# Optimization experiments

Hardware: AMD Instinct MI355X
Metric: run time of the kernel (lower is better)

## Reference

```python
import jax, jax.numpy as jnp
import numpy as np


def setup_inputs() -> dict:
    key = jax.random.key(0)
    ks = jax.random.split(key, 7)
    N, E, D_IN, D_OUT = 50000, 800000, 128, 128
    features = jax.random.normal(ks[0], (N, D_IN), dtype=jnp.float32)
    src = jax.random.randint(ks[1], (E,), 0, N, dtype=jnp.int64)
    dst = jax.random.randint(ks[2], (E,), 0, N, dtype=jnp.int64)
    W1 = jax.random.normal(ks[3], (D_OUT, D_IN), dtype=jnp.float32) * (1.0 / np.sqrt(D_IN))
    b1 = jax.random.normal(ks[4], (D_OUT,), dtype=jnp.float32) * 0.01
    W2 = jax.random.normal(ks[5], (1, 2 * D_OUT), dtype=jnp.float32) * (1.0 / np.sqrt(2 * D_OUT))
    b2 = jax.random.normal(ks[6], (1,), dtype=jnp.float32) * 0.01
    return {"features": features, "src": src, "dst": dst,
            "W1": W1, "b1": b1, "W2": W2, "b2": b2}


def reference(features, src, dst, W1, b1, W2, b2):
    # Gather endpoint features per edge: [E, D_in]
    f_src = features[src]
    f_dst = features[dst]
    # Shared linear projection (torch Linear: x @ W.T + b) -> [E, D_out]
    h_src = jnp.einsum('ed,od->eo', f_src, W1) + b1
    h_dst = jnp.einsum('ed,od->eo', f_dst, W1) + b1
    # Concat [diff, sum] -> [E, 2*D_out]; dropout is identity at inference
    e_feats = jnp.concatenate([h_src - h_dst, h_src + h_dst], axis=1)
    # Final linear to scalar per edge, squeeze, tanh -> [E]
    out = jnp.tanh((jnp.einsum('ef,of->eo', e_feats, W2) + b2).squeeze(-1))
    return out
```

## Files before the change

kernel.cpp:

```cpp
#include <hip/hip_runtime.h>
#include <math.h>

#define D 128


__global__ void prep_kernel(const float* __restrict__ W1, const float* __restrict__ b1,
                            const float* __restrict__ W2, const float* __restrict__ b2,
                            float* __restrict__ uvc) {
    __shared__ float su[4 * D];
    __shared__ float sv[4 * D];
    __shared__ float sc[D];
    int tid = threadIdx.x;
    int d = tid & (D - 1);
    int ch = tid >> 7;
    float u = 0.f, v = 0.f;
    int o0 = ch * 32;
    #pragma unroll 8
    for (int k = 0; k < 32; ++k) {
        int o = o0 + k;
        float wa = W2[o];
        float wb = W2[D + o];
        float w1 = W1[o * D + d];
        u += (wa + wb) * w1;
        v += (wb - wa) * w1;
    }
    su[ch * D + d] = u;
    sv[ch * D + d] = v;
    if (ch == 0) sc[d] = 2.f * W2[D + d] * b1[d];
    __syncthreads();
    if (tid < D) {
        float uu = su[d] + su[D + d] + su[2 * D + d] + su[3 * D + d];
        float vv = sv[d] + sv[D + d] + sv[2 * D + d] + sv[3 * D + d];
        uvc[2 * d]     = uu;
        uvc[2 * d + 1] = vv;
    } else if (tid == D) {
        float cc = b2[0];
        for (int o = 0; o < D; ++o) cc += sc[o];
        uvc[2 * D] = cc;
    }
}

__global__ void node_kernel(const float* __restrict__ feat, const float* __restrict__ uvc,
                            float2* __restrict__ st, int N) {
    int wave = (int)((blockIdx.x * blockDim.x + threadIdx.x) >> 6);
    int lane = threadIdx.x & 63;
    int half = lane >> 5;
    int l = lane & 31;
    int node = wave * 2 + half;
    if (node >= N) return;
    float4 f = ((const float4*)(feat + (size_t)node * D))[l];
    float4 a = ((const float4*)uvc)[2 * l];
    float4 b = ((const float4*)uvc)[2 * l + 1];
    float s = f.x * a.x + f.y * a.z + f.z * b.x + f.w * b.z;
    float t = f.x * a.y + f.y * a.w + f.z * b.y + f.w * b.w;
    #pragma unroll
    for (int off = 16; off; off >>= 1) {
        s += __shfl_xor(s, off, 64);
        t += __shfl_xor(t, off, 64);
    }
    if (l == 0) st[node] = make_float2(s, t);
}

__global__ void edge_kernel(const int* __restrict__ src, const int* __restrict__ dst,
                            const float2* __restrict__ st, const float* __restrict__ uvc,
                            float* __restrict__ out, int E) {
    int i = blockIdx.x * blockDim.x + threadIdx.x;
    int e0 = i * 4;
    if (e0 >= E) return;
    float c = uvc[2 * D];
    if (e0 + 3 < E) {
        int4 si = ((const int4*)src)[i];
        int4 di = ((const int4*)dst)[i];
        float2 a0 = st[si.x], a1 = st[si.y], a2 = st[si.z], a3 = st[si.w];
        float2 b0 = st[di.x], b1v = st[di.y], b2v = st[di.z], b3 = st[di.w];
        float4 r;
        r.x = tanhf(a0.x + b0.y + c);
        r.y = tanhf(a1.x + b1v.y + c);
        r.z = tanhf(a2.x + b2v.y + c);
        r.w = tanhf(a3.x + b3.y + c);
        ((float4*)out)[i] = r;
    } else {
        for (int e = e0; e < E; ++e)
            out[e] = tanhf(st[src[e]].x + st[dst[e]].y + c);
    }
}

__global__ void fused_edge_kernel(const float* __restrict__ feat,
                                  const int* __restrict__ src, const int* __restrict__ dst,
                                  const float* __restrict__ uvc, float* __restrict__ out, int E) {
    int wave = (int)((blockIdx.x * blockDim.x + threadIdx.x) >> 6);
    int lane = threadIdx.x & 63;
    if (wave >= E) return;
    int sn = src[wave], dn = dst[wave];
    float2 fs = ((const float2*)(feat + (size_t)sn * D))[lane];
    float2 fd = ((const float2*)(feat + (size_t)dn * D))[lane];
    float2 p = ((const float2*)uvc)[2 * lane];
    float2 q = ((const float2*)uvc)[2 * lane + 1];
    float acc = fs.x * p.x + fs.y * q.x + fd.x * p.y + fd.y * q.y;
    #pragma unroll
    for (int off = 32; off; off >>= 1) acc += __shfl_xor(acc, off, 64);
    if (lane == 0) out[wave] = tanhf(acc + uvc[2 * D]);
}

extern "C" void kernel_launch(void* const* d_in, const int* in_sizes, int n_in,
                              void* d_out, int out_size, void* d_ws, size_t ws_size,
                              hipStream_t stream) {
    const float* feat = (const float*)d_in[0];
    const int*   src  = (const int*)d_in[1];
    const int*   dst  = (const int*)d_in[2];
    const float* W1   = (const float*)d_in[3];
    const float* b1   = (const float*)d_in[4];
    const float* W2   = (const float*)d_in[5];
    const float* b2   = (const float*)d_in[6];
    float* out = (float*)d_out;

    int N = in_sizes[0] / D;
    int E = in_sizes[1];

    float* uvc = (float*)d_ws;
    float2* st = (float2*)((float*)d_ws + 512);
    size_t needed = (512 + 2 * (size_t)N) * sizeof(float);

    prep_kernel<<<1, 512, 0, stream>>>(W1, b1, W2, b2, uvc);

    if (ws_size >= needed) {
        int nblocks = (N + 7) / 8;
        node_kernel<<<nblocks, 256, 0, stream>>>(feat, uvc, st, N);
        int nthreads = (E + 3) / 4;
        edge_kernel<<<(nthreads + 255) / 256, 256, 0, stream>>>(src, dst, st, uvc, out, E);
    } else {
        int nblocks = (E + 3) / 4;
        fused_edge_kernel<<<nblocks, 256, 0, stream>>>(feat, src, dst, uvc, out, E);
    }
}
```

Baseline: 95.13 us.

## Fuse weight-folding prep into persistent node kernel and fold bias into node scores

Removes the separate single-block prep kernel launch by having every block of a grid-stride node kernel redundantly compute the folded u/v vectors and bias constant in shared memory. The bias constant is added into the per-node source score, so the edge kernel no longer reads it. The node kernel becomes persistent with at most 512 blocks. The tradeoff is that each block redoes the 128x128 weight fold, about 64 KB of W1 reads per block, which should mostly be served from cache.

```diff
diff --git a/kernel.cpp b/kernel.cpp
--- a/kernel.cpp
+++ b/kernel.cpp
@@ -3,6 +3,84 @@
 
 #define D 128
 
+
+__global__ void __launch_bounds__(256) node_fused_kernel(
+        const float* __restrict__ W1, const float* __restrict__ b1,
+        const float* __restrict__ W2, const float* __restrict__ b2,
+        const float* __restrict__ feat, float2* __restrict__ st, int N) {
+    __shared__ float uv[2 * D + 2];
+    __shared__ float red[2 * D];
+    __shared__ float csc[D];
+    int tid = threadIdx.x;
+    int d = tid & (D - 1);
+    int ch = tid >> 7;
+    float u = 0.f, v = 0.f;
+    int o0 = ch * 64;
+    #pragma unroll 16
+    for (int k = 0; k < 64; ++k) {
+        int o = o0 + k;
+        float wa = W2[o];
+        float wb = W2[D + o];
+        float w1 = W1[o * D + d];
+        u += (wa + wb) * w1;
+        v += (wb - wa) * w1;
+    }
+    if (ch == 0) { red[d] = u; red[D + d] = v; csc[d] = 2.f * W2[D + d] * b1[d]; }
+    __syncthreads();
+    if (ch == 1) {
+        uv[2 * d]     = red[d] + u;
+        uv[2 * d + 1] = red[D + d] + v;
+    }
+    if (tid == 0) {
+        float cc = b2[0];
+        #pragma unroll 16
+        for (int o = 0; o < D; ++o) cc += csc[o];
+        uv[2 * D] = cc;
+    }
+    __syncthreads();
+    float c = uv[2 * D];
+
+    int lane = tid & 63;
+    int half = lane >> 5;
+    int l = lane & 31;
+    int waveInBlock = tid >> 6;
+    int stride = gridDim.x * 8;
+    float4 a = ((const float4*)uv)[2 * l];
+    float4 b = ((const float4*)uv)[2 * l + 1];
+    for (int node = blockIdx.x * 8 + waveInBlock * 2 + half; node < N; node += stride) {
+        float4 f = ((const float4*)(feat + (size_t)node * D))[l];
+        float s = f.x * a.x + f.y * a.z + f.z * b.x + f.w * b.z;
+        float t = f.x * a.y + f.y * a.w + f.z * b.y + f.w * b.w;
+        #pragma unroll
+        for (int off = 16; off; off >>= 1) {
+            s += __shfl_xor(s, off, 64);
+            t += __shfl_xor(t, off, 64);
+        }
+        if (l == 0) st[node] = make_float2(s + c, t);
+    }
+}
+
+__global__ void edge_kernel(const int* __restrict__ src, const int* __restrict__ dst,
+                            const float2* __restrict__ st, float* __restrict__ out, int E) {
+    int i = blockIdx.x * blockDim.x + threadIdx.x;
+    int e0 = i * 4;
+    if (e0 >= E) return;
+    if (e0 + 3 < E) {
+        int4 si = ((const int4*)src)[i];
+        int4 di = ((const int4*)dst)[i];
+        float2 a0 = st[si.x], a1 = st[si.y], a2 = st[si.z], a3 = st[si.w];
+        float2 b0 = st[di.x], b1v = st[di.y], b2v = st[di.z], b3 = st[di.w];
+        float4 r;
+        r.x = tanhf(a0.x + b0.y);
+        r.y = tanhf(a1.x + b1v.y);
+        r.z = tanhf(a2.x + b2v.y);
+        r.w = tanhf(a3.x + b3.y);
+        ((float4*)out)[i] = r;
+    } else {
+        for (int e = e0; e < E; ++e)
+            out[e] = tanhf(st[src[e]].x + st[dst[e]].y);
+    }
+}
 
 __global__ void prep_kernel(const float* __restrict__ W1, const float* __restrict__ b1,
                             const float* __restrict__ W2, const float* __restrict__ b2,
@@ -29,59 +107,12 @@
     if (ch == 0) sc[d] = 2.f * W2[D + d] * b1[d];
     __syncthreads();
     if (tid < D) {
-        float uu = su[d] + su[D + d] + su[2 * D + d] + su[3 * D + d];
-        float vv = sv[d] + sv[D + d] + sv[2 * D + d] + sv[3 * D + d];
-        uvc[2 * d]     = uu;
-        uvc[2 * d + 1] = vv;
+        uvc[2 * d]     = su[d] + su[D + d] + su[2 * D + d] + su[3 * D + d];
+        uvc[2 * d + 1] = sv[d] + sv[D + d] + sv[2 * D + d] + sv[3 * D + d];
     } else if (tid == D) {
         float cc = b2[0];
         for (int o = 0; o < D; ++o) cc += sc[o];
         uvc[2 * D] = cc;
-    }
-}
-
-__global__ void node_kernel(const float* __restrict__ feat, const float* __restrict__ uvc,
-                            float2* __restrict__ st, int N) {
-    int wave = (int)((blockIdx.x * blockDim.x + threadIdx.x) >> 6);
-    int lane = threadIdx.x & 63;
-    int half = lane >> 5;
-    int l = lane & 31;
-    int node = wave * 2 + half;
-    if (node >= N) return;
-    float4 f = ((const float4*)(feat + (size_t)node * D))[l];
-    float4 a = ((const float4*)uvc)[2 * l];
-    float4 b = ((const float4*)uvc)[2 * l + 1];
-    float s = f.x * a.x + f.y * a.z + f.z * b.x + f.w * b.z;
-    float t = f.x * a.y + f.y * a.w + f.z * b.y + f.w * b.w;
-    #pragma unroll
-    for (int off = 16; off; off >>= 1) {
-        s += __shfl_xor(s, off, 64);
-        t += __shfl_xor(t, off, 64);
-    }
-    if (l == 0) st[node] = make_float2(s, t);
-}
-
-__global__ void edge_kernel(const int* __restrict__ src, const int* __restrict__ dst,
-                            const float2* __restrict__ st, const float* __restrict__ uvc,
-                            float* __restrict__ out, int E) {
-    int i = blockIdx.x * blockDim.x + threadIdx.x;
-    int e0 = i * 4;
-    if (e0 >= E) return;
-    float c = uvc[2 * D];
-    if (e0 + 3 < E) {
-        int4 si = ((const int4*)src)[i];
-        int4 di = ((const int4*)dst)[i];
-        float2 a0 = st[si.x], a1 = st[si.y], a2 = st[si.z], a3 = st[si.w];
-        float2 b0 = st[di.x], b1v = st[di.y], b2v = st[di.z], b3 = st[di.w];
-        float4 r;
-        r.x = tanhf(a0.x + b0.y + c);
-        r.y = tanhf(a1.x + b1v.y + c);
-        r.z = tanhf(a2.x + b2v.y + c);
-        r.w = tanhf(a3.x + b3.y + c);
-        ((float4*)out)[i] = r;
-    } else {
-        for (int e = e0; e < E; ++e)
-            out[e] = tanhf(st[src[e]].x + st[dst[e]].y + c);
     }
 }
 
@@ -117,18 +148,18 @@
     int N = in_sizes[0] / D;
     int E = in_sizes[1];
 
-    float* uvc = (float*)d_ws;
-    float2* st = (float2*)((float*)d_ws + 512);
-    size_t needed = (512 + 2 * (size_t)N) * sizeof(float);
-
-    prep_kernel<<<1, 512, 0, stream>>>(W1, b1, W2, b2, uvc);
+    size_t needed = 2 * (size_t)N * sizeof(float);
 
     if (ws_size >= needed) {
-        int nblocks = (N + 7) / 8;
-        node_kernel<<<nblocks, 256, 0, stream>>>(feat, uvc, st, N);
+        float2* st = (float2*)d_ws;
+        int nblocks = 512;
+        if (nblocks > (N + 7) / 8) nblocks = (N + 7) / 8;
+        node_fused_kernel<<<nblocks, 256, 0, stream>>>(W1, b1, W2, b2, feat, st, N);
         int nthreads = (E + 3) / 4;
-        edge_kernel<<<(nthreads + 255) / 256, 256, 0, stream>>>(src, dst, st, uvc, out, E);
+        edge_kernel<<<(nthreads + 255) / 256, 256, 0, stream>>>(src, dst, st, out, E);
     } else {
+        float* uvc = (float*)d_ws;
+        prep_kernel<<<1, 512, 0, stream>>>(W1, b1, W2, b2, uvc);
         int nblocks = (E + 3) / 4;
         fused_edge_kernel<<<nblocks, 256, 0, stream>>>(feat, src, dst, uvc, out, E);
     }
```

After: 98.85 us. 1.04x slower.
